# Optimization experiments

Measured on AMD Instinct MI355X. Metric: run time of the kernel, lower is better.

Reference implementation:

```python
import jax, jax.numpy as jnp
import numpy as np

D_MODEL = 2048
N_HEADS = 16
QK_ROPE = 64
QK_NOPE = 128
KV_LORA = 512
V_DIM = 128
QK_DIM = QK_ROPE + QK_NOPE
RMS_EPS = 1.1920928955078125e-07  # torch fp32 finfo.eps (nn.RMSNorm default eps=None)


def apply_rope(x, base=10000.0):
    # x: [B, S, H, D] ; torchtune-style interleaved-pair rotary
    B, S, H, D = x.shape
    freqs = 1.0 / (base ** (jnp.arange(0, D, 2, dtype=jnp.float32) / D))  # [D/2]
    t = jnp.arange(S, dtype=jnp.float32)[:, None] * freqs[None, :]        # [S, D/2]
    cos = jnp.cos(t)[None, :, None, :]
    sin = jnp.sin(t)[None, :, None, :]
    x1 = x[..., 0::2]
    x2 = x[..., 1::2]
    out = jnp.stack([x1 * cos - x2 * sin, x2 * cos + x1 * sin], axis=-1)
    return out.reshape(B, S, H, D).astype(x.dtype)


def setup_inputs() -> dict:
    key = jax.random.key(0)
    ks = jax.random.split(key, 6)
    s = lambda fan_in: 1.0 / np.sqrt(fan_in)
    x = jax.random.normal(ks[0], (2, 2048, D_MODEL), dtype=jnp.float32)
    Wq = jax.random.normal(ks[1], (D_MODEL, N_HEADS * QK_DIM), dtype=jnp.float32) * s(D_MODEL)
    Wkv_a = jax.random.normal(ks[2], (D_MODEL, KV_LORA + QK_ROPE), dtype=jnp.float32) * s(D_MODEL)
    kv_norm_w = jnp.ones((KV_LORA,), dtype=jnp.float32)
    Wkv_b = jax.random.normal(ks[3], (KV_LORA, N_HEADS * (QK_NOPE + V_DIM)), dtype=jnp.float32) * s(KV_LORA)
    Wo = jax.random.normal(ks[4], (N_HEADS * V_DIM, D_MODEL), dtype=jnp.float32) * s(N_HEADS * V_DIM)
    return {"x": x, "Wq": Wq, "Wkv_a": Wkv_a, "kv_norm_w": kv_norm_w, "Wkv_b": Wkv_b, "Wo": Wo}


def reference(x, Wq, Wkv_a, kv_norm_w, Wkv_b, Wo):
    B, S, _ = x.shape
    # queries: split nope/rope, rotary on rope slice only
    q = (x @ Wq).reshape(B, S, N_HEADS, QK_DIM)
    q_nope, q_rope = q[..., :QK_NOPE], q[..., QK_NOPE:]
    q = jnp.concatenate([q_nope, apply_rope(q_rope)], axis=-1)  # [B,S,H,QK_DIM]
    # compressed kv + decoupled rope key
    kv = x @ Wkv_a                                              # [B,S,KV_LORA+QK_ROPE]
    c_kv, k_rope = kv[..., :KV_LORA], kv[..., KV_LORA:]
    k_rope = apply_rope(k_rope.reshape(B, S, 1, QK_ROPE))       # [B,S,1,QK_ROPE]
    # RMSNorm on compressed latent, then decompress
    c_kv = c_kv * jax.lax.rsqrt(jnp.mean(c_kv * c_kv, axis=-1, keepdims=True) + RMS_EPS) * kv_norm_w
    kv = (c_kv @ Wkv_b).reshape(B, S, N_HEADS, QK_NOPE + V_DIM)
    k_nope, v = kv[..., :QK_NOPE], kv[..., QK_NOPE:]
    k = jnp.concatenate([k_nope, jnp.broadcast_to(k_rope, (B, S, N_HEADS, QK_ROPE))], axis=-1)
    # causal SDPA over sequence dim
    scale = 1.0 / np.sqrt(QK_DIM)
    scores = jnp.einsum('bqhd,bkhd->bhqk', q, k) * scale        # [B,H,S,S]
    mask = jnp.tril(jnp.ones((S, S), dtype=bool))
    scores = jnp.where(mask, scores, jnp.finfo(scores.dtype).min)
    attn = jax.nn.softmax(scores, axis=-1)
    out = jnp.einsum('bhqk,bkhd->bqhd', attn, v).reshape(B, S, N_HEADS * V_DIM)
    return out @ Wo
```

## Files before the change

kernel.cpp:

```cpp
#include <hip/hip_runtime.h>
#include <hip/hip_bf16.h>
#include <math.h>

#define BATCH   2
#define SEQ     2048
#define DM      2048
#define NH      16
#define QKR     64
#define QKN     128
#define KVL     512
#define VD      128
#define QKD     192
#define KVA_LD  640
#define RMS_EPS 1.1920928955078125e-07f

typedef __bf16 bf16x8 __attribute__((ext_vector_type(8)));
typedef float  f32x4  __attribute__((ext_vector_type(4)));

__device__ __forceinline__ void async16(const __bf16* g, __bf16* l)
{
    __builtin_amdgcn_global_load_lds(
        (__attribute__((address_space(1))) unsigned int*)g,
        (__attribute__((address_space(3))) unsigned int*)l,
        16, 0, 0);
}

template<int CTRL>
__device__ __forceinline__ float dppf(float x)
{
    int y = __builtin_amdgcn_update_dpp(0, __builtin_bit_cast(int, x), CTRL, 0xF, 0xF, false);
    return __builtin_bit_cast(float, y);
}

__global__ __launch_bounds__(256) void f32_to_bf16(const float* __restrict__ src,
                                                   __bf16* __restrict__ dst)
{
    int i = (blockIdx.x * 256 + threadIdx.x) * 4;
    float4 v = *reinterpret_cast<const float4*>(src + i);
    dst[i + 0] = (__bf16)v.x;
    dst[i + 1] = (__bf16)v.y;
    dst[i + 2] = (__bf16)v.z;
    dst[i + 3] = (__bf16)v.w;
}

__global__ __launch_bounds__(256) void transpose_w(const float* __restrict__ W,
                                                   __bf16* __restrict__ Wt,
                                                   int K, int N)
{
    __shared__ float t[64][65];
    const int n0 = blockIdx.x * 64, k0 = blockIdx.y * 64;
    const int tid = threadIdx.x;
    #pragma unroll
    for (int i = 0; i < 16; ++i) {
        int flat = i * 256 + tid;
        int kl = flat >> 6, nl = flat & 63;
        t[kl][nl] = (n0 + nl < N) ? W[(size_t)(k0 + kl) * N + n0 + nl] : 0.f;
    }
    __syncthreads();
    #pragma unroll
    for (int i = 0; i < 16; ++i) {
        int flat = i * 256 + tid;
        int nl = flat >> 6, kl = flat & 63;
        Wt[(size_t)(n0 + nl) * K + k0 + kl] = (__bf16)t[kl][nl];
    }
}

template<typename OT>
__global__ __launch_bounds__(256) void gemm_bf16(const __bf16* __restrict__ A,
                                                 const __bf16* __restrict__ Bt,
                                                 OT* __restrict__ C,
                                                 int K, int lda, int ldb, int ldc)
{
    __shared__ __bf16 As[128 * 64];
    __shared__ __bf16 Bs[128 * 64];
    const int tid = threadIdx.x;
    const int lane = tid & 63, wave = tid >> 6;
    const int n = lane & 15, quad = lane >> 4;
    const int row0 = blockIdx.y * 128, col0 = blockIdx.x * 128;
    const int wm = (wave >> 1) * 64, wn = (wave & 1) * 64;

    f32x4 acc[4][4];
    #pragma unroll
    for (int mi = 0; mi < 4; ++mi)
        #pragma unroll
        for (int ni = 0; ni < 4; ++ni)
            #pragma unroll
            for (int r = 0; r < 4; ++r) acc[mi][ni][r] = 0.f;

    const int srow = tid >> 3;
    const int scol8p = tid & 7;
    const __bf16* Ag[4]; const __bf16* Bg[4];
    #pragma unroll
    for (int i = 0; i < 4; ++i) {
        int row = srow + i * 32;
        int col8l = scol8p ^ (row & 7);
        Ag[i] = A  + (size_t)(row0 + row) * lda + col8l * 8;
        Bg[i] = Bt + (size_t)(col0 + row) * ldb + col8l * 8;
    }
    __bf16* Asd = As + tid * 8;
    __bf16* Bsd = Bs + tid * 8;

    for (int k0 = 0; k0 < K; k0 += 64) {
        __syncthreads();
        #pragma unroll
        for (int i = 0; i < 4; ++i) {
            async16(Ag[i] + k0, Asd + i * 2048);
            async16(Bg[i] + k0, Bsd + i * 2048);
        }
        __syncthreads();

        #pragma unroll
        for (int kc = 0; kc < 2; ++kc) {
            bf16x8 af[4], bfr[4];
            #pragma unroll
            for (int mi = 0; mi < 4; ++mi) {
                int row = wm + mi * 16 + n;
                int slot = (kc * 4 + quad) ^ (row & 7);
                af[mi] = *reinterpret_cast<const bf16x8*>(&As[row * 64 + slot * 8]);
            }
            #pragma unroll
            for (int ni = 0; ni < 4; ++ni) {
                int row = wn + ni * 16 + n;
                int slot = (kc * 4 + quad) ^ (row & 7);
                bfr[ni] = *reinterpret_cast<const bf16x8*>(&Bs[row * 64 + slot * 8]);
            }
            #pragma unroll
            for (int mi = 0; mi < 4; ++mi)
                #pragma unroll
                for (int ni = 0; ni < 4; ++ni)
                    acc[mi][ni] = __builtin_amdgcn_mfma_f32_16x16x32_bf16(af[mi], bfr[ni], acc[mi][ni], 0, 0, 0);
        }
    }

    #pragma unroll
    for (int mi = 0; mi < 4; ++mi)
        #pragma unroll
        for (int r = 0; r < 4; ++r) {
            OT* cp = C + (size_t)(row0 + wm + mi * 16 + quad * 4 + r) * ldc + col0 + wn + n;
            #pragma unroll
            for (int ni = 0; ni < 4; ++ni)
                cp[ni * 16] = (OT)acc[mi][ni][r];
        }
}

__global__ __launch_bounds__(256) void rope_q_kernel(__bf16* __restrict__ q)
{
    int idx = blockIdx.x * 256 + threadIdx.x;
    int i = idx & 31;
    int h = (idx >> 5) & 15;
    int s = (idx >> 9) & 2047;
    int b = idx >> 20;
    float t = (float)s * __expf(-(float)(2 * i) / 64.0f * 9.210340371976184f);
    float c = __cosf(t), sn = __sinf(t);
    __bf16* p = q + ((size_t)(b * SEQ + s)) * (NH * QKD) + h * QKD + QKN + 2 * i;
    float x1 = (float)p[0], x2 = (float)p[1];
    p[0] = (__bf16)(x1 * c - x2 * sn);
    p[1] = (__bf16)(x2 * c + x1 * sn);
}

__global__ __launch_bounds__(256) void rope_k_kernel(const float* __restrict__ kva,
                                                     __bf16* __restrict__ krope)
{
    int idx = blockIdx.x * 256 + threadIdx.x;
    int i = idx & 31;
    int s = (idx >> 5) & 2047;
    int b = idx >> 16;
    float t = (float)s * __expf(-(float)(2 * i) / 64.0f * 9.210340371976184f);
    float c = __cosf(t), sn = __sinf(t);
    const float* p = kva + ((size_t)(b * SEQ + s)) * KVA_LD + KVL + 2 * i;
    float x1 = p[0], x2 = p[1];
    __bf16* o = krope + ((size_t)(b * SEQ + s)) * QKR + 2 * i;
    o[0] = (__bf16)(x1 * c - x2 * sn);
    o[1] = (__bf16)(x2 * c + x1 * sn);
}

__global__ __launch_bounds__(256) void rmsnorm_kernel(const float* __restrict__ kva,
                                                      const float* __restrict__ w,
                                                      __bf16* __restrict__ out)
{
    const int rid = blockIdx.x;
    const float* row = kva + (size_t)rid * KVA_LD;
    const int tid = threadIdx.x;
    float v[2];
    float ss = 0.f;
    #pragma unroll
    for (int j = 0; j < 2; ++j) {
        int d = tid + j * 256;
        v[j] = row[d];
        ss += v[j] * v[j];
    }
    #pragma unroll
    for (int off = 32; off > 0; off >>= 1) ss += __shfl_down(ss, off, 64);
    __shared__ float red[4];
    if ((tid & 63) == 0) red[tid >> 6] = ss;
    __syncthreads();
    float total = red[0] + red[1] + red[2] + red[3];
    float scale = 1.0f / sqrtf(total * (1.0f / KVL) + RMS_EPS);
    #pragma unroll
    for (int j = 0; j < 2; ++j) {
        int d = tid + j * 256;
        out[(size_t)rid * KVL + d] = (__bf16)(v[j] * scale * w[d]);
    }
}

__global__ __launch_bounds__(256) void build_vt(const __bf16* __restrict__ kvb,
                                                __bf16* __restrict__ Vt)
{
    __shared__ __bf16 tile[64][136];
    const int s0 = blockIdx.x * 64, h = blockIdx.y, b = blockIdx.z;
    const int t = threadIdx.x;
    #pragma unroll
    for (int i = 0; i < 4; ++i) {
        int flat = i * 256 + t;
        int sl = flat >> 4, c8 = flat & 15;
        bf16x8 v = *reinterpret_cast<const bf16x8*>(
            &kvb[((size_t)(b * SEQ + s0 + sl)) * (NH * 256) + h * 256 + 128 + c8 * 8]);
        *reinterpret_cast<bf16x8*>(&tile[sl][c8 * 8]) = v;
    }
    __syncthreads();
    #pragma unroll
    for (int j = 0; j < 32; ++j) {
        int flat = j * 256 + t;
        int d = flat >> 6, sl = flat & 63;
        Vt[((size_t)((b * NH + h) * VD + d)) * SEQ + s0 + sl] = tile[sl][d];
    }
}

#define LKS 200
#define LVS 72
#define LPS 72
__global__ __launch_bounds__(256, 2) void attn_mfma(const __bf16* __restrict__ qb,
                                                    const __bf16* __restrict__ kvb,
                                                    const __bf16* __restrict__ krope,
                                                    const __bf16* __restrict__ Vt,
                                                    __bf16* __restrict__ ob)
{
    __shared__ __bf16 Ks[64 * LKS];
    __shared__ __bf16 Vs[128 * LVS];
    __shared__ __bf16 Ps[4 * 16 * LPS];
    const int tid = threadIdx.x;
    const int wave = tid >> 6, lane = tid & 63;
    const int n = lane & 15, quad = lane >> 4;
    const int pair = blockIdx.x, h = blockIdx.y, b = blockIdx.z;
    const int bh = b * NH + h;
    const float scale = 0.07216878364870323f;
    int qs[2];
    qs[0] = pair; qs[1] = 31 - pair;
    const int ntmax = qs[1] + 1;

    const __bf16 one_bf = (__bf16)1.0f;
    const bf16x8 onesf = {one_bf, one_bf, one_bf, one_bf, one_bf, one_bf, one_bf, one_bf};

    bf16x8 qfrag[2][6];
    #pragma unroll
    for (int s = 0; s < 2; ++s) {
        const int qrow = qs[s] * 64 + wave * 16 + n;
        const __bf16* qp = qb + ((size_t)(b * SEQ + qrow)) * (NH * QKD) + h * QKD + quad * 8;
        #pragma unroll
        for (int c = 0; c < 6; ++c)
            qfrag[s][c] = *reinterpret_cast<const bf16x8*>(qp + c * 32);
    }

    f32x4 Oa[2][8];
    f32x4 Ol[2];
    float m_i[2][4];
    #pragma unroll
    for (int s = 0; s < 2; ++s) {
        #pragma unroll
        for (int i = 0; i < 8; ++i)
            #pragma unroll
            for (int r = 0; r < 4; ++r) Oa[s][i][r] = 0.f;
        #pragma unroll
        for (int r = 0; r < 4; ++r) { Ol[s][r] = 0.f; m_i[s][r] = -1e30f; }
    }

    int kkey[6], kc8[6];
    #pragma unroll
    for (int i = 0; i < 6; ++i) {
        int flat = i * 256 + tid;
        kkey[i] = flat / 24; kc8[i] = flat % 24;
    }
    const int vd = tid >> 3, vc8 = tid & 7;

    const __bf16* Vg = Vt + (size_t)bh * VD * SEQ;

    bf16x8 kpre[6], vpre[4];
    {
        const int k0 = 0;
        #pragma unroll
        for (int i = 0; i < 6; ++i) {
            const __bf16* src = (kc8[i] < 16)
                ? kvb + ((size_t)(b * SEQ + k0 + kkey[i])) * (NH * 256) + h * 256 + kc8[i] * 8
                : krope + ((size_t)(b * SEQ + k0 + kkey[i])) * QKR + (kc8[i] - 16) * 8;
            kpre[i] = *reinterpret_cast<const bf16x8*>(src);
        }
        #pragma unroll
        for (int i = 0; i < 4; ++i)
            vpre[i] = *reinterpret_cast<const bf16x8*>(Vg + (size_t)(vd + i * 32) * SEQ + k0 + vc8 * 8);
    }

    for (int kt = 0; kt < ntmax; ++kt) {
        __syncthreads();
        #pragma unroll
        for (int i = 0; i < 6; ++i)
            *reinterpret_cast<bf16x8*>(&Ks[kkey[i] * LKS + kc8[i] * 8]) = kpre[i];
        #pragma unroll
        for (int i = 0; i < 4; ++i)
            *reinterpret_cast<bf16x8*>(&Vs[(vd + i * 32) * LVS + vc8 * 8]) = vpre[i];
        __syncthreads();

        if (kt + 1 < ntmax) {
            const int k0n = (kt + 1) * 64;
            #pragma unroll
            for (int i = 0; i < 6; ++i) {
                const __bf16* src = (kc8[i] < 16)
                    ? kvb + ((size_t)(b * SEQ + k0n + kkey[i])) * (NH * 256) + h * 256 + kc8[i] * 8
                    : krope + ((size_t)(b * SEQ + k0n + kkey[i])) * QKR + (kc8[i] - 16) * 8;
                kpre[i] = *reinterpret_cast<const bf16x8*>(src);
            }
            #pragma unroll
            for (int i = 0; i < 4; ++i)
                vpre[i] = *reinterpret_cast<const bf16x8*>(Vg + (size_t)(vd + i * 32) * SEQ + k0n + vc8 * 8);
        }

        const int k0 = kt * 64;
        #pragma unroll
        for (int s = 0; s < 2; ++s) {
            if (kt > qs[s]) continue;

            f32x4 sacc[4];
            #pragma unroll
            for (int t = 0; t < 4; ++t) {
                f32x4 a;
                #pragma unroll
                for (int r = 0; r < 4; ++r) a[r] = 0.f;
                #pragma unroll
                for (int c = 0; c < 6; ++c) {
                    bf16x8 kf = *reinterpret_cast<const bf16x8*>(&Ks[(t * 16 + n) * LKS + c * 32 + quad * 8]);
                    a = __builtin_amdgcn_mfma_f32_16x16x32_bf16(qfrag[s][c], kf, a, 0, 0, 0);
                }
                sacc[t] = a;
            }

            const int qg = qs[s] * 64 + wave * 16 + quad * 4;
            const bool diag = (kt == qs[s]);
            float mloc[4];
            #pragma unroll
            for (int r = 0; r < 4; ++r) mloc[r] = -1e30f;
            #pragma unroll
            for (int t = 0; t < 4; ++t) {
                int key = k0 + t * 16 + n;
                #pragma unroll
                for (int r = 0; r < 4; ++r) {
                    float sv = sacc[t][r] * scale;
                    if (diag) sv = (key <= qg + r) ? sv : -1e30f;
                    sacc[t][r] = sv;
                    mloc[r] = fmaxf(mloc[r], sv);
                }
            }
            #pragma unroll
            for (int r = 0; r < 4; ++r) mloc[r] = fmaxf(mloc[r], dppf<0x121>(mloc[r]));
            #pragma unroll
            for (int r = 0; r < 4; ++r) mloc[r] = fmaxf(mloc[r], dppf<0x122>(mloc[r]));
            #pragma unroll
            for (int r = 0; r < 4; ++r) mloc[r] = fmaxf(mloc[r], dppf<0x124>(mloc[r]));
            #pragma unroll
            for (int r = 0; r < 4; ++r) mloc[r] = fmaxf(mloc[r], dppf<0x128>(mloc[r]));

            float mnew[4];
            #pragma unroll
            for (int r = 0; r < 4; ++r) mnew[r] = fmaxf(m_i[s][r], mloc[r]);
            int grow = __any((mnew[0] > m_i[s][0]) || (mnew[1] > m_i[s][1]) ||
                             (mnew[2] > m_i[s][2]) || (mnew[3] > m_i[s][3]));
            if (grow) {
                float alpha[4];
                #pragma unroll
                for (int r = 0; r < 4; ++r) alpha[r] = __expf(m_i[s][r] - mnew[r]);
                #pragma unroll
                for (int i = 0; i < 8; ++i)
                    #pragma unroll
                    for (int r = 0; r < 4; ++r) Oa[s][i][r] *= alpha[r];
                #pragma unroll
                for (int r = 0; r < 4; ++r) Ol[s][r] *= alpha[r];
            }
            #pragma unroll
            for (int r = 0; r < 4; ++r) m_i[s][r] = mnew[r];

            #pragma unroll
            for (int t = 0; t < 4; ++t)
                #pragma unroll
                for (int r = 0; r < 4; ++r) {
                    float p = __expf(sacc[t][r] - m_i[s][r]);
                    Ps[wave * 16 * LPS + (quad * 4 + r) * LPS + t * 16 + n] = (__bf16)p;
                }

            __asm__ volatile("s_waitcnt lgkmcnt(0)" ::: "memory");

            #pragma unroll
            for (int kc = 0; kc < 2; ++kc) {
                bf16x8 pf = *reinterpret_cast<const bf16x8*>(&Ps[wave * 16 * LPS + n * LPS + kc * 32 + quad * 8]);
                Ol[s] = __builtin_amdgcn_mfma_f32_16x16x32_bf16(pf, onesf, Ol[s], 0, 0, 0);
                #pragma unroll
                for (int vt = 0; vt < 8; ++vt) {
                    bf16x8 vf = *reinterpret_cast<const bf16x8*>(&Vs[(vt * 16 + n) * LVS + kc * 32 + quad * 8]);
                    Oa[s][vt] = __builtin_amdgcn_mfma_f32_16x16x32_bf16(pf, vf, Oa[s][vt], 0, 0, 0);
                }
            }
        }
    }

    #pragma unroll
    for (int s = 0; s < 2; ++s)
        #pragma unroll
        for (int r = 0; r < 4; ++r) {
            float inv = 1.0f / Ol[s][r];
            int row = qs[s] * 64 + wave * 16 + quad * 4 + r;
            __bf16* op = ob + ((size_t)(b * SEQ + row)) * (NH * VD) + h * VD;
            #pragma unroll
            for (int vt = 0; vt < 8; ++vt)
                op[vt * 16 + n] = (__bf16)(Oa[s][vt][r] * inv);
        }
}

extern "C" void kernel_launch(void* const* d_in, const int* in_sizes, int n_in,
                              void* d_out, int out_size, void* d_ws, size_t ws_size,
                              hipStream_t stream)
{
    const float* x         = (const float*)d_in[0];
    const float* Wq        = (const float*)d_in[1];
    const float* Wkv_a     = (const float*)d_in[2];
    const float* kv_norm_w = (const float*)d_in[3];
    const float* Wkv_b     = (const float*)d_in[4];
    const float* Wo        = (const float*)d_in[5];
    float* out = (float*)d_out;

    float* ws = (float*)d_ws;
    __bf16* q_bf   = (__bf16*)ws;
    float*  kv_a   = ws + 6291456;
    __bf16* kv_b   = (__bf16*)(ws + 8912896);
    float*  r3     = ws + 17301504;
    __bf16* xb     = (__bf16*)r3;
    __bf16* Vt     = (__bf16*)r3;
    float*  r4     = ws + 21495808;
    __bf16* Wq_t   = (__bf16*)r4;
    __bf16* Wkva_t = (__bf16*)(r4 + 3145728);
    __bf16* Wkvb_t = (__bf16*)(r4 + 3801088);
    __bf16* attn_o = (__bf16*)r4;
    __bf16* Wo_t   = (__bf16*)(ws + 27787264);
    __bf16* c_kv_n = (__bf16*)(ws + 29884416);
    __bf16* krope  = (__bf16*)(ws + 30932992);

    const int M = BATCH * SEQ;
    dim3 blk(256);

    f32_to_bf16<<<(M * DM) / 1024, blk, 0, stream>>>(x, xb);
    transpose_w<<<dim3(3072 / 64, 2048 / 64), blk, 0, stream>>>(Wq, Wq_t, DM, NH * QKD);
    transpose_w<<<dim3(640 / 64, 2048 / 64), blk, 0, stream>>>(Wkv_a, Wkva_t, DM, KVL + QKR);
    transpose_w<<<dim3(4096 / 64, 512 / 64), blk, 0, stream>>>(Wkv_b, Wkvb_t, KVL, NH * 256);
    transpose_w<<<dim3(2048 / 64, 2048 / 64), blk, 0, stream>>>(Wo, Wo_t, NH * VD, DM);

    gemm_bf16<__bf16><<<dim3(3072 / 128, M / 128), blk, 0, stream>>>(xb, Wq_t, q_bf, DM, DM, DM, NH * QKD);
    gemm_bf16<float><<<dim3(640 / 128, M / 128), blk, 0, stream>>>(xb, Wkva_t, kv_a, DM, DM, DM, KVA_LD);

    rope_q_kernel<<<(BATCH * SEQ * NH * 32) / 256, blk, 0, stream>>>(q_bf);
    rope_k_kernel<<<(BATCH * SEQ * 32) / 256, blk, 0, stream>>>(kv_a, krope);
    rmsnorm_kernel<<<M, blk, 0, stream>>>(kv_a, kv_norm_w, c_kv_n);

    gemm_bf16<__bf16><<<dim3(4096 / 128, M / 128), blk, 0, stream>>>(c_kv_n, Wkvb_t, kv_b, KVL, KVL, KVL, NH * 256);

    build_vt<<<dim3(SEQ / 64, NH, BATCH), blk, 0, stream>>>(kv_b, Vt);

    attn_mfma<<<dim3(16, NH, BATCH), blk, 0, stream>>>(q_bf, kv_b, krope, Vt, attn_o);

    gemm_bf16<float><<<dim3(2048 / 128, M / 128), blk, 0, stream>>>(attn_o, Wo_t, out, NH * VD, NH * VD, NH * VD, DM);
}
```

Before: 449.9 us.

## Reassign attention waves to strips with shared K fragments; fuse small prep kernels

Attention waves are reassigned: each pair of waves now owns one query strip with 32 rows per wave, instead of every wave covering 16 rows of both strips. Each K fragment read from LDS then feeds two MFMAs, and each V fragment likewise, which cuts LDS reads per MFMA. The P buffer in LDS doubles, and waves on the short strip finish early, so work inside a block is less balanced. Separately, the input conversion and the four weight transposes are merged into one launch, and q-rope, k-rope and RMSNorm into another, to cut launch overhead.

```diff
diff --git a/kernel.cpp b/kernel.cpp
--- a/kernel.cpp
+++ b/kernel.cpp
@@ -32,24 +32,36 @@
     return __builtin_bit_cast(float, y);
 }
 
-__global__ __launch_bounds__(256) void f32_to_bf16(const float* __restrict__ src,
-                                                   __bf16* __restrict__ dst)
-{
-    int i = (blockIdx.x * 256 + threadIdx.x) * 4;
-    float4 v = *reinterpret_cast<const float4*>(src + i);
-    dst[i + 0] = (__bf16)v.x;
-    dst[i + 1] = (__bf16)v.y;
-    dst[i + 2] = (__bf16)v.z;
-    dst[i + 3] = (__bf16)v.w;
-}
-
-__global__ __launch_bounds__(256) void transpose_w(const float* __restrict__ W,
-                                                   __bf16* __restrict__ Wt,
-                                                   int K, int N)
+__global__ __launch_bounds__(256) void prep_kernel(const float* __restrict__ x,
+                                                   __bf16* __restrict__ xb,
+                                                   const float* __restrict__ Wq,
+                                                   __bf16* __restrict__ Wq_t,
+                                                   const float* __restrict__ Wkv_a,
+                                                   __bf16* __restrict__ Wkva_t,
+                                                   const float* __restrict__ Wkv_b,
+                                                   __bf16* __restrict__ Wkvb_t,
+                                                   const float* __restrict__ Wo,
+                                                   __bf16* __restrict__ Wo_t)
 {
     __shared__ float t[64][65];
-    const int n0 = blockIdx.x * 64, k0 = blockIdx.y * 64;
     const int tid = threadIdx.x;
+    int id = blockIdx.x;
+    if (id < 8192) {
+        int i = (id * 256 + tid) * 4;
+        float4 v = *reinterpret_cast<const float4*>(x + i);
+        xb[i + 0] = (__bf16)v.x;
+        xb[i + 1] = (__bf16)v.y;
+        xb[i + 2] = (__bf16)v.z;
+        xb[i + 3] = (__bf16)v.w;
+        return;
+    }
+    id -= 8192;
+    const float* W; __bf16* Wt; int K, N, nb;
+    if (id < 1536)      {            W = Wq;    Wt = Wq_t;   K = 2048; N = 3072; nb = 48; }
+    else if (id < 1856) { id -= 1536; W = Wkv_a; Wt = Wkva_t; K = 2048; N = 576;  nb = 10; }
+    else if (id < 2368) { id -= 1856; W = Wkv_b; Wt = Wkvb_t; K = 512;  N = 4096; nb = 64; }
+    else                { id -= 2368; W = Wo;    Wt = Wo_t;   K = 2048; N = 2048; nb = 32; }
+    const int n0 = (id % nb) * 64, k0 = (id / nb) * 64;
     #pragma unroll
     for (int i = 0; i < 16; ++i) {
         int flat = i * 256 + tid;
@@ -143,44 +155,44 @@
         }
 }
 
-__global__ __launch_bounds__(256) void rope_q_kernel(__bf16* __restrict__ q)
-{
-    int idx = blockIdx.x * 256 + threadIdx.x;
-    int i = idx & 31;
-    int h = (idx >> 5) & 15;
-    int s = (idx >> 9) & 2047;
-    int b = idx >> 20;
-    float t = (float)s * __expf(-(float)(2 * i) / 64.0f * 9.210340371976184f);
-    float c = __cosf(t), sn = __sinf(t);
-    __bf16* p = q + ((size_t)(b * SEQ + s)) * (NH * QKD) + h * QKD + QKN + 2 * i;
-    float x1 = (float)p[0], x2 = (float)p[1];
-    p[0] = (__bf16)(x1 * c - x2 * sn);
-    p[1] = (__bf16)(x2 * c + x1 * sn);
-}
-
-__global__ __launch_bounds__(256) void rope_k_kernel(const float* __restrict__ kva,
-                                                     __bf16* __restrict__ krope)
-{
-    int idx = blockIdx.x * 256 + threadIdx.x;
-    int i = idx & 31;
-    int s = (idx >> 5) & 2047;
-    int b = idx >> 16;
-    float t = (float)s * __expf(-(float)(2 * i) / 64.0f * 9.210340371976184f);
-    float c = __cosf(t), sn = __sinf(t);
-    const float* p = kva + ((size_t)(b * SEQ + s)) * KVA_LD + KVL + 2 * i;
-    float x1 = p[0], x2 = p[1];
-    __bf16* o = krope + ((size_t)(b * SEQ + s)) * QKR + 2 * i;
-    o[0] = (__bf16)(x1 * c - x2 * sn);
-    o[1] = (__bf16)(x2 * c + x1 * sn);
-}
-
-__global__ __launch_bounds__(256) void rmsnorm_kernel(const float* __restrict__ kva,
-                                                      const float* __restrict__ w,
-                                                      __bf16* __restrict__ out)
-{
-    const int rid = blockIdx.x;
+__global__ __launch_bounds__(256) void post1_kernel(__bf16* __restrict__ q,
+                                                    const float* __restrict__ kva,
+                                                    const float* __restrict__ w,
+                                                    __bf16* __restrict__ ckv,
+                                                    __bf16* __restrict__ krope)
+{
+    const int tid = threadIdx.x;
+    int id = blockIdx.x;
+    if (id < 8192) {
+        int idx = id * 256 + tid;
+        int i = idx & 31;
+        int h = (idx >> 5) & 15;
+        int s = (idx >> 9) & 2047;
+        int b = idx >> 20;
+        float t = (float)s * __expf(-(float)(2 * i) / 64.0f * 9.210340371976184f);
+        float c = __cosf(t), sn = __sinf(t);
+        __bf16* p = q + ((size_t)(b * SEQ + s)) * (NH * QKD) + h * QKD + QKN + 2 * i;
+        float x1 = (float)p[0], x2 = (float)p[1];
+        p[0] = (__bf16)(x1 * c - x2 * sn);
+        p[1] = (__bf16)(x2 * c + x1 * sn);
+        return;
+    }
+    if (id < 8704) {
+        int idx = (id - 8192) * 256 + tid;
+        int i = idx & 31;
+        int s = (idx >> 5) & 2047;
+        int b = idx >> 16;
+        float t = (float)s * __expf(-(float)(2 * i) / 64.0f * 9.210340371976184f);
+        float c = __cosf(t), sn = __sinf(t);
+        const float* p = kva + ((size_t)(b * SEQ + s)) * KVA_LD + KVL + 2 * i;
+        float x1 = p[0], x2 = p[1];
+        __bf16* o = krope + ((size_t)(b * SEQ + s)) * QKR + 2 * i;
+        o[0] = (__bf16)(x1 * c - x2 * sn);
+        o[1] = (__bf16)(x2 * c + x1 * sn);
+        return;
+    }
+    const int rid = id - 8704;
     const float* row = kva + (size_t)rid * KVA_LD;
-    const int tid = threadIdx.x;
     float v[2];
     float ss = 0.f;
     #pragma unroll
@@ -199,7 +211,7 @@
     #pragma unroll
     for (int j = 0; j < 2; ++j) {
         int d = tid + j * 256;
-        out[(size_t)rid * KVL + d] = (__bf16)(v[j] * scale * w[d]);
+        ckv[(size_t)rid * KVL + d] = (__bf16)(v[j] * scale * w[d]);
     }
 }
 
@@ -237,41 +249,42 @@
 {
     __shared__ __bf16 Ks[64 * LKS];
     __shared__ __bf16 Vs[128 * LVS];
-    __shared__ __bf16 Ps[4 * 16 * LPS];
+    __shared__ __bf16 Ps[8 * 16 * LPS];
     const int tid = threadIdx.x;
     const int wave = tid >> 6, lane = tid & 63;
     const int n = lane & 15, quad = lane >> 4;
     const int pair = blockIdx.x, h = blockIdx.y, b = blockIdx.z;
     const int bh = b * NH + h;
     const float scale = 0.07216878364870323f;
-    int qs[2];
-    qs[0] = pair; qs[1] = 31 - pair;
-    const int ntmax = qs[1] + 1;
+    const int qs1 = 31 - pair;
+    const int mystrip = (wave >> 1) ? qs1 : pair;
+    const int whalf = wave & 1;
+    const int ntmax = qs1 + 1;
 
     const __bf16 one_bf = (__bf16)1.0f;
     const bf16x8 onesf = {one_bf, one_bf, one_bf, one_bf, one_bf, one_bf, one_bf, one_bf};
 
     bf16x8 qfrag[2][6];
     #pragma unroll
-    for (int s = 0; s < 2; ++s) {
-        const int qrow = qs[s] * 64 + wave * 16 + n;
+    for (int qt = 0; qt < 2; ++qt) {
+        const int qrow = mystrip * 64 + whalf * 32 + qt * 16 + n;
         const __bf16* qp = qb + ((size_t)(b * SEQ + qrow)) * (NH * QKD) + h * QKD + quad * 8;
         #pragma unroll
         for (int c = 0; c < 6; ++c)
-            qfrag[s][c] = *reinterpret_cast<const bf16x8*>(qp + c * 32);
+            qfrag[qt][c] = *reinterpret_cast<const bf16x8*>(qp + c * 32);
     }
 
     f32x4 Oa[2][8];
     f32x4 Ol[2];
     float m_i[2][4];
     #pragma unroll
-    for (int s = 0; s < 2; ++s) {
+    for (int qt = 0; qt < 2; ++qt) {
         #pragma unroll
         for (int i = 0; i < 8; ++i)
             #pragma unroll
-            for (int r = 0; r < 4; ++r) Oa[s][i][r] = 0.f;
-        #pragma unroll
-        for (int r = 0; r < 4; ++r) { Ol[s][r] = 0.f; m_i[s][r] = -1e30f; }
+            for (int r = 0; r < 4; ++r) Oa[qt][i][r] = 0.f;
+        #pragma unroll
+        for (int r = 0; r < 4; ++r) { Ol[qt][r] = 0.f; m_i[qt][r] = -1e30f; }
     }
 
     int kkey[6], kc8[6];
@@ -323,102 +336,108 @@
                 vpre[i] = *reinterpret_cast<const bf16x8*>(Vg + (size_t)(vd + i * 32) * SEQ + k0n + vc8 * 8);
         }
 
-        const int k0 = kt * 64;
-        #pragma unroll
-        for (int s = 0; s < 2; ++s) {
-            if (kt > qs[s]) continue;
-
-            f32x4 sacc[4];
-            #pragma unroll
-            for (int t = 0; t < 4; ++t) {
-                f32x4 a;
-                #pragma unroll
-                for (int r = 0; r < 4; ++r) a[r] = 0.f;
+        if (kt <= mystrip) {
+            const int k0 = kt * 64;
+
+            f32x4 sacc[2][4];
+            #pragma unroll
+            for (int qt = 0; qt < 2; ++qt)
+                #pragma unroll
+                for (int t = 0; t < 4; ++t)
+                    #pragma unroll
+                    for (int r = 0; r < 4; ++r) sacc[qt][t][r] = 0.f;
+            #pragma unroll
+            for (int t = 0; t < 4; ++t)
                 #pragma unroll
                 for (int c = 0; c < 6; ++c) {
                     bf16x8 kf = *reinterpret_cast<const bf16x8*>(&Ks[(t * 16 + n) * LKS + c * 32 + quad * 8]);
-                    a = __builtin_amdgcn_mfma_f32_16x16x32_bf16(qfrag[s][c], kf, a, 0, 0, 0);
+                    sacc[0][t] = __builtin_amdgcn_mfma_f32_16x16x32_bf16(qfrag[0][c], kf, sacc[0][t], 0, 0, 0);
+                    sacc[1][t] = __builtin_amdgcn_mfma_f32_16x16x32_bf16(qfrag[1][c], kf, sacc[1][t], 0, 0, 0);
                 }
-                sacc[t] = a;
+
+            const bool diag = (kt == mystrip);
+            #pragma unroll
+            for (int qt = 0; qt < 2; ++qt) {
+                const int qg = mystrip * 64 + whalf * 32 + qt * 16 + quad * 4;
+                float mloc[4];
+                #pragma unroll
+                for (int r = 0; r < 4; ++r) mloc[r] = -1e30f;
+                #pragma unroll
+                for (int t = 0; t < 4; ++t) {
+                    int key = k0 + t * 16 + n;
+                    #pragma unroll
+                    for (int r = 0; r < 4; ++r) {
+                        float sv = sacc[qt][t][r] * scale;
+                        if (diag) sv = (key <= qg + r) ? sv : -1e30f;
+                        sacc[qt][t][r] = sv;
+                        mloc[r] = fmaxf(mloc[r], sv);
+                    }
+                }
+                #pragma unroll
+                for (int r = 0; r < 4; ++r) mloc[r] = fmaxf(mloc[r], dppf<0x121>(mloc[r]));
+                #pragma unroll
+                for (int r = 0; r < 4; ++r) mloc[r] = fmaxf(mloc[r], dppf<0x122>(mloc[r]));
+                #pragma unroll
+                for (int r = 0; r < 4; ++r) mloc[r] = fmaxf(mloc[r], dppf<0x124>(mloc[r]));
+                #pragma unroll
+                for (int r = 0; r < 4; ++r) mloc[r] = fmaxf(mloc[r], dppf<0x128>(mloc[r]));
+
+                float mnew[4];
+                #pragma unroll
+                for (int r = 0; r < 4; ++r) mnew[r] = fmaxf(m_i[qt][r], mloc[r]);
+                int grow = __any((mnew[0] > m_i[qt][0]) || (mnew[1] > m_i[qt][1]) ||
+                                 (mnew[2] > m_i[qt][2]) || (mnew[3] > m_i[qt][3]));
+                if (grow) {
+                    float alpha[4];
+                    #pragma unroll
+                    for (int r = 0; r < 4; ++r) alpha[r] = __expf(m_i[qt][r] - mnew[r]);
+                    #pragma unroll
+                    for (int i = 0; i < 8; ++i)
+                        #pragma unroll
+                        for (int r = 0; r < 4; ++r) Oa[qt][i][r] *= alpha[r];
+                    #pragma unroll
+                    for (int r = 0; r < 4; ++r) Ol[qt][r] *= alpha[r];
+                }
+                #pragma unroll
+                for (int r = 0; r < 4; ++r) m_i[qt][r] = mnew[r];
+
+                #pragma unroll
+                for (int t = 0; t < 4; ++t)
+                    #pragma unroll
+                    for (int r = 0; r < 4; ++r) {
+                        float p = __expf(sacc[qt][t][r] - m_i[qt][r]);
+                        Ps[wave * 32 * LPS + (qt * 16 + quad * 4 + r) * LPS + t * 16 + n] = (__bf16)p;
+                    }
             }
 
-            const int qg = qs[s] * 64 + wave * 16 + quad * 4;
-            const bool diag = (kt == qs[s]);
-            float mloc[4];
-            #pragma unroll
-            for (int r = 0; r < 4; ++r) mloc[r] = -1e30f;
-            #pragma unroll
-            for (int t = 0; t < 4; ++t) {
-                int key = k0 + t * 16 + n;
-                #pragma unroll
-                for (int r = 0; r < 4; ++r) {
-                    float sv = sacc[t][r] * scale;
-                    if (diag) sv = (key <= qg + r) ? sv : -1e30f;
-                    sacc[t][r] = sv;
-                    mloc[r] = fmaxf(mloc[r], sv);
+            __asm__ volatile("s_waitcnt lgkmcnt(0)" ::: "memory");
+
+            #pragma unroll
+            for (int kc = 0; kc < 2; ++kc) {
+                bf16x8 pf0 = *reinterpret_cast<const bf16x8*>(&Ps[wave * 32 * LPS + n * LPS + kc * 32 + quad * 8]);
+                bf16x8 pf1 = *reinterpret_cast<const bf16x8*>(&Ps[wave * 32 * LPS + (16 + n) * LPS + kc * 32 + quad * 8]);
+                Ol[0] = __builtin_amdgcn_mfma_f32_16x16x32_bf16(pf0, onesf, Ol[0], 0, 0, 0);
+                Ol[1] = __builtin_amdgcn_mfma_f32_16x16x32_bf16(pf1, onesf, Ol[1], 0, 0, 0);
+                #pragma unroll
+                for (int vt = 0; vt < 8; ++vt) {
+                    bf16x8 vf = *reinterpret_cast<const bf16x8*>(&Vs[(vt * 16 + n) * LVS + kc * 32 + quad * 8]);
+                    Oa[0][vt] = __builtin_amdgcn_mfma_f32_16x16x32_bf16(pf0, vf, Oa[0][vt], 0, 0, 0);
+                    Oa[1][vt] = __builtin_amdgcn_mfma_f32_16x16x32_bf16(pf1, vf, Oa[1][vt], 0, 0, 0);
                 }
             }
-            #pragma unroll
-            for (int r = 0; r < 4; ++r) mloc[r] = fmaxf(mloc[r], dppf<0x121>(mloc[r]));
-            #pragma unroll
-            for (int r = 0; r < 4; ++r) mloc[r] = fmaxf(mloc[r], dppf<0x122>(mloc[r]));
-            #pragma unroll
-            for (int r = 0; r < 4; ++r) mloc[r] = fmaxf(mloc[r], dppf<0x124>(mloc[r]));
-            #pragma unroll
-            for (int r = 0; r < 4; ++r) mloc[r] = fmaxf(mloc[r], dppf<0x128>(mloc[r]));
-
-            float mnew[4];
-            #pragma unroll
-            for (int r = 0; r < 4; ++r) mnew[r] = fmaxf(m_i[s][r], mloc[r]);
-            int grow = __any((mnew[0] > m_i[s][0]) || (mnew[1] > m_i[s][1]) ||
-                             (mnew[2] > m_i[s][2]) || (mnew[3] > m_i[s][3]));
-            if (grow) {
-                float alpha[4];
-                #pragma unroll
-                for (int r = 0; r < 4; ++r) alpha[r] = __expf(m_i[s][r] - mnew[r]);
-                #pragma unroll
-                for (int i = 0; i < 8; ++i)
-                    #pragma unroll
-                    for (int r = 0; r < 4; ++r) Oa[s][i][r] *= alpha[r];
-                #pragma unroll
-                for (int r = 0; r < 4; ++r) Ol[s][r] *= alpha[r];
-            }
-            #pragma unroll
-            for (int r = 0; r < 4; ++r) m_i[s][r] = mnew[r];
-
-            #pragma unroll
-            for (int t = 0; t < 4; ++t)
-                #pragma unroll
-                for (int r = 0; r < 4; ++r) {
-                    float p = __expf(sacc[t][r] - m_i[s][r]);
-                    Ps[wave * 16 * LPS + (quad * 4 + r) * LPS + t * 16 + n] = (__bf16)p;
-                }
-
-            __asm__ volatile("s_waitcnt lgkmcnt(0)" ::: "memory");
-
-            #pragma unroll
-            for (int kc = 0; kc < 2; ++kc) {
-                bf16x8 pf = *reinterpret_cast<const bf16x8*>(&Ps[wave * 16 * LPS + n * LPS + kc * 32 + quad * 8]);
-                Ol[s] = __builtin_amdgcn_mfma_f32_16x16x32_bf16(pf, onesf, Ol[s], 0, 0, 0);
-                #pragma unroll
-                for (int vt = 0; vt < 8; ++vt) {
-                    bf16x8 vf = *reinterpret_cast<const bf16x8*>(&Vs[(vt * 16 + n) * LVS + kc * 32 + quad * 8]);
-                    Oa[s][vt] = __builtin_amdgcn_mfma_f32_16x16x32_bf16(pf, vf, Oa[s][vt], 0, 0, 0);
-                }
-            }
-        }
-    }
-
-    #pragma unroll
-    for (int s = 0; s < 2; ++s)
+        }
+    }
+
+    #pragma unroll
+    for (int qt = 0; qt < 2; ++qt)
         #pragma unroll
         for (int r = 0; r < 4; ++r) {
-            float inv = 1.0f / Ol[s][r];
-            int row = qs[s] * 64 + wave * 16 + quad * 4 + r;
+            float inv = 1.0f / Ol[qt][r];
+            int row = mystrip * 64 + whalf * 32 + qt * 16 + quad * 4 + r;
             __bf16* op = ob + ((size_t)(b * SEQ + row)) * (NH * VD) + h * VD;
             #pragma unroll
             for (int vt = 0; vt < 8; ++vt)
-                op[vt * 16 + n] = (__bf16)(Oa[s][vt][r] * inv);
+                op[vt * 16 + n] = (__bf16)(Oa[qt][vt][r] * inv);
         }
 }
 
@@ -453,18 +472,13 @@
     const int M = BATCH * SEQ;
     dim3 blk(256);
 
-    f32_to_bf16<<<(M * DM) / 1024, blk, 0, stream>>>(x, xb);
-    transpose_w<<<dim3(3072 / 64, 2048 / 64), blk, 0, stream>>>(Wq, Wq_t, DM, NH * QKD);
-    transpose_w<<<dim3(640 / 64, 2048 / 64), blk, 0, stream>>>(Wkv_a, Wkva_t, DM, KVL + QKR);
-    transpose_w<<<dim3(4096 / 64, 512 / 64), blk, 0, stream>>>(Wkv_b, Wkvb_t, KVL, NH * 256);
-    transpose_w<<<dim3(2048 / 64, 2048 / 64), blk, 0, stream>>>(Wo, Wo_t, NH * VD, DM);
+    prep_kernel<<<11584, blk, 0, stream>>>(x, xb, Wq, Wq_t, Wkv_a, Wkva_t,
+                                           Wkv_b, Wkvb_t, Wo, Wo_t);
 
     gemm_bf16<__bf16><<<dim3(3072 / 128, M / 128), blk, 0, stream>>>(xb, Wq_t, q_bf, DM, DM, DM, NH * QKD);
     gemm_bf16<float><<<dim3(640 / 128, M / 128), blk, 0, stream>>>(xb, Wkva_t, kv_a, DM, DM, DM, KVA_LD);
 
-    rope_q_kernel<<<(BATCH * SEQ * NH * 32) / 256, blk, 0, stream>>>(q_bf);
-    rope_k_kernel<<<(BATCH * SEQ * 32) / 256, blk, 0, stream>>>(kv_a, krope);
-    rmsnorm_kernel<<<M, blk, 0, stream>>>(kv_a, kv_norm_w, c_kv_n);
+    post1_kernel<<<12800, blk, 0, stream>>>(q_bf, kv_a, kv_norm_w, c_kv_n, krope);
 
     gemm_bf16<__bf16><<<dim3(4096 / 128, M / 128), blk, 0, stream>>>(c_kv_n, Wkvb_t, kv_b, KVL, KVL, KVL, NH * 256);
 
```

After: 487.4 us. 8.3% more time.
